# Optimization experiments

Measured on AMD Instinct MI355X. Metric: run time of the kernel, lower is better.

Reference implementation:

```python
import jax, jax.numpy as jnp
import numpy as np

N, P, M, J, H = 32768, 5, 1024, 24, 256
SMPL_THRESH = 0.08


def _rand_transforms(rng, n):
    # random small-angle rotations + small translations -> invertible 4x4 joint transforms
    axis = rng.normal(size=(n, 3))
    axis /= np.linalg.norm(axis, axis=-1, keepdims=True)
    ang = rng.uniform(-0.5, 0.5, size=(n, 1, 1))
    K = np.zeros((n, 3, 3))
    K[:, 0, 1] = -axis[:, 2]; K[:, 0, 2] = axis[:, 1]
    K[:, 1, 0] = axis[:, 2];  K[:, 1, 2] = -axis[:, 0]
    K[:, 2, 0] = -axis[:, 1]; K[:, 2, 1] = axis[:, 0]
    R = np.eye(3)[None] + np.sin(ang) * K + (1.0 - np.cos(ang)) * (K @ K)
    T = np.zeros((n, 4, 4))
    T[:, :3, :3] = R
    T[:, :3, 3] = rng.normal(size=(n, 3)) * 0.1
    T[:, 3, 3] = 1.0
    return T.astype(np.float32)


def setup_inputs() -> dict:
    key = jax.random.key(0)
    ks = jax.random.split(key, 12)
    rng = np.random.default_rng(0)
    pose_pts = jax.random.normal(ks[0], (1, N, 3), jnp.float32) * 0.5
    pose_dirs = jax.random.normal(ks[1], (1, N, 3), jnp.float32)
    pose_dirs = pose_dirs / jnp.linalg.norm(pose_dirs, axis=-1, keepdims=True)
    part_pts = jax.random.normal(ks[2], (P, M, 3), jnp.float32) * 0.5
    part_pbw = jax.nn.softmax(jax.random.normal(ks[3], (P, M, J), jnp.float32), axis=-1)
    A = jnp.asarray(_rand_transforms(rng, J))[None]       # [1,24,4,4]
    big_A = jnp.asarray(_rand_transforms(rng, J))[None]   # [1,24,4,4]
    W1 = jax.random.normal(ks[4], (3, H), jnp.float32) * 0.1
    b1 = jnp.zeros((H,), jnp.float32)
    W2 = jax.random.normal(ks[5], (H, H), jnp.float32) * 0.06
    b2 = jnp.zeros((H,), jnp.float32)
    W3 = jax.random.normal(ks[6], (H, 3), jnp.float32) * 0.06
    b3 = jnp.zeros((3,), jnp.float32)
    lengths2 = jnp.full((P,), M, dtype=jnp.int32)
    return {"pose_pts": pose_pts, "pose_dirs": pose_dirs, "part_pts": part_pts,
            "part_pbw": part_pbw, "A": A, "big_A": big_A,
            "W1": W1, "b1": b1, "W2": W2, "b2": b2, "W3": W3, "b3": b3,
            "lengths2": lengths2}


def _lbs_pipeline(pose_pts, pose_dirs, part_pts, part_pbw, A, big_A,
                  W1, b1, W2, b2, W3, b3, lengths2):
    # ---- KNN (K=1) blend-weight lookup per part (torch.no_grad block) ----
    x = pose_pts[0]                                              # [N,3]
    d2 = (jnp.sum(x * x, -1)[:, None, None]
          - 2.0 * jnp.einsum('nd,pmd->npm', x, part_pts)
          + jnp.sum(part_pts * part_pts, -1)[None])              # [N,P,M]
    valid = jnp.arange(M)[None, :] < lengths2[:, None]           # [P,M]
    d2 = jnp.where(valid[None], jnp.maximum(d2, 0.0), jnp.inf)
    nn = jnp.argmin(d2, axis=-1)                                 # [N,P]
    pnorm = jnp.sqrt(jnp.take_along_axis(d2, nn[..., None], -1)[..., 0])  # [N,P]
    bw = part_pbw[jnp.arange(P)[None, :], nn]                    # [N,P,24]
    bw = jax.lax.stop_gradient(bw)
    pnorm = jax.lax.stop_gradient(pnorm)
    pflag = pnorm < SMPL_THRESH                                  # [N,P]

    # ---- gather-expand: each point assigned to every part ----
    pts_e = jnp.broadcast_to(x[:, None, :], (N, P, 3)).reshape(N * P, 3)
    dirs_e = jnp.broadcast_to(pose_dirs[0][:, None, :], (N, P, 3)).reshape(N * P, 3)
    bw_f = bw.reshape(N * P, J)

    # ---- per-point inverse linear blend skinning ----
    A_bw = jnp.einsum('kj,jxy->kxy', bw_f, A[0])                 # [NP,4,4]
    R_inv = jnp.linalg.inv(A_bw[:, :3, :3])
    tpts = jnp.einsum('kxy,ky->kx', R_inv, pts_e - A_bw[:, :3, 3])
    Ab = jnp.einsum('kj,jxy->kxy', bw_f, big_A[0])               # [NP,4,4]
    Rb = Ab[:, :3, :3]
    init_bigpose = jnp.einsum('kxy,ky->kx', Rb, tpts) + Ab[:, :3, 3]
    tdirs = jnp.einsum('kxy,ky->kx', R_inv, dirs_e)
    tpose_dirs = jnp.einsum('kxy,ky->kx', Rb, tdirs).reshape(1, N, P, 3)

    # ---- tpose deformer (residual MLP, masked by part flag) ----
    h = jax.nn.relu(init_bigpose @ W1 + b1)
    h = jax.nn.relu(h @ W2 + b2)
    resd = 0.05 * jnp.tanh(h @ W3 + b3)
    resd = resd * pflag.reshape(N * P, 1).astype(resd.dtype)
    tpose = (init_bigpose + resd).reshape(1, N, P, 3)
    return (tpose, tpose_dirs, resd.reshape(1, N, P, 3),
            pflag.reshape(1, N, P), init_bigpose[None], pnorm[None])


def reference(pose_pts, pose_dirs, part_pts, part_pbw, A, big_A,
              W1, b1, W2, b2, W3, b3, lengths2):
    return _lbs_pipeline(pose_pts, pose_dirs, part_pts, part_pbw, A, big_A,
                         W1, b1, W2, b2, W3, b3, lengths2)
```

## Files before the change

### kernel.cpp

```cpp
#include <hip/hip_runtime.h>
#include <stdint.h>
#include <math.h>

#define NPTS 32768
#define PP   5
#define MM   1024
#define JJ   24
#define HH   256

#define O0 0
#define O1 491520
#define O2 983040
#define O3 1474560
#define O4 1638400
#define O5 2129920

typedef unsigned short ushort_t;
typedef unsigned int   uint_t;
typedef unsigned long long u64_t;
typedef __attribute__((ext_vector_type(8))) short bf16x8;
typedef __attribute__((ext_vector_type(4))) float f32x4;
typedef __attribute__((ext_vector_type(2))) float f32x2;

__device__ __forceinline__ ushort_t f2bf(float f) {
  union { uint_t i; float f; } v; v.f = f;
  uint_t i = v.i;
  return (ushort_t)((i + 0x7FFFu + ((i >> 16) & 1u)) >> 16);
}
__device__ __forceinline__ uint_t cvt_pk_bf16(float lo, float hi) {
  uint_t r;
  asm("v_cvt_pk_bf16_f32 %0, %1, %2" : "=v"(r) : "v"(lo), "v"(hi));
  return r;
}
__device__ __forceinline__ float tanh_fast(float v) {
  v = fminf(fmaxf(v, -15.f), 15.f);
  float e = __expf(2.f*v);
  return __fdividef(e - 1.f, e + 1.f);
}
__device__ __forceinline__ float dpp_sum16(float x) {
  x += __int_as_float(__builtin_amdgcn_update_dpp(0, __float_as_int(x), 0x108, 0xF, 0xF, true));
  x += __int_as_float(__builtin_amdgcn_update_dpp(0, __float_as_int(x), 0x104, 0xF, 0xF, true));
  x += __int_as_float(__builtin_amdgcn_update_dpp(0, __float_as_int(x), 0x102, 0xF, 0xF, true));
  x += __int_as_float(__builtin_amdgcn_update_dpp(0, __float_as_int(x), 0x101, 0xF, 0xF, true));
  return x;
}

__device__ __forceinline__ void transform_one(
    int n, int p, int nn, float pn, float fl,
    float px, float py, float pz, float dx, float dy, float dz,
    const float* __restrict__ pbw,
    const float4* __restrict__ sA4, const float4* __restrict__ sB4,
    float* __restrict__ out)
{
  const float4* bwr = (const float4*)(pbw + ((size_t)p * MM + nn) * JJ);
  float bw[24];
  #pragma unroll
  for (int q = 0; q < 6; ++q) {
    float4 u = bwr[q];
    bw[q*4+0] = u.x; bw[q*4+1] = u.y; bw[q*4+2] = u.z; bw[q*4+3] = u.w;
  }

  float M1[12], M2[12];
  #pragma unroll
  for (int q = 0; q < 12; ++q) { M1[q] = 0.f; M2[q] = 0.f; }
  #pragma unroll
  for (int j = 0; j < 24; ++j) {
    float w = bw[j];
    float4 a0 = sA4[j*3+0], a1 = sA4[j*3+1], a2 = sA4[j*3+2];
    M1[0]=fmaf(w,a0.x,M1[0]); M1[1]=fmaf(w,a0.y,M1[1]); M1[2]=fmaf(w,a0.z,M1[2]); M1[3]=fmaf(w,a0.w,M1[3]);
    M1[4]=fmaf(w,a1.x,M1[4]); M1[5]=fmaf(w,a1.y,M1[5]); M1[6]=fmaf(w,a1.z,M1[6]); M1[7]=fmaf(w,a1.w,M1[7]);
    M1[8]=fmaf(w,a2.x,M1[8]); M1[9]=fmaf(w,a2.y,M1[9]); M1[10]=fmaf(w,a2.z,M1[10]); M1[11]=fmaf(w,a2.w,M1[11]);
    float4 c0 = sB4[j*3+0], c1 = sB4[j*3+1], c2 = sB4[j*3+2];
    M2[0]=fmaf(w,c0.x,M2[0]); M2[1]=fmaf(w,c0.y,M2[1]); M2[2]=fmaf(w,c0.z,M2[2]); M2[3]=fmaf(w,c0.w,M2[3]);
    M2[4]=fmaf(w,c1.x,M2[4]); M2[5]=fmaf(w,c1.y,M2[5]); M2[6]=fmaf(w,c1.z,M2[6]); M2[7]=fmaf(w,c1.w,M2[7]);
    M2[8]=fmaf(w,c2.x,M2[8]); M2[9]=fmaf(w,c2.y,M2[9]); M2[10]=fmaf(w,c2.z,M2[10]); M2[11]=fmaf(w,c2.w,M2[11]);
  }
  float a=M1[0], b=M1[1], c=M1[2];
  float d=M1[4], e=M1[5], f=M1[6];
  float g=M1[8], h=M1[9], i=M1[10];
  float C00 = e*i - f*h, C01 = c*h - b*i, C02 = b*f - c*e;
  float C10 = f*g - d*i, C11 = a*i - c*g, C12 = c*d - a*f;
  float C20 = d*h - e*g, C21 = b*g - a*h, C22 = a*e - b*d;
  float det = a*C00 + b*C10 + c*C20;
  float rd = 1.0f / det;
  float tx = px - M1[3], ty = py - M1[7], tz = pz - M1[11];
  float t0 = rd * (C00*tx + C01*ty + C02*tz);
  float t1 = rd * (C10*tx + C11*ty + C12*tz);
  float t2 = rd * (C20*tx + C21*ty + C22*tz);
  float i0 = M2[0]*t0 + M2[1]*t1 + M2[2]*t2  + M2[3];
  float i1 = M2[4]*t0 + M2[5]*t1 + M2[6]*t2  + M2[7];
  float i2 = M2[8]*t0 + M2[9]*t1 + M2[10]*t2 + M2[11];
  float d0 = rd * (C00*dx + C01*dy + C02*dz);
  float d1 = rd * (C10*dx + C11*dy + C12*dz);
  float d2 = rd * (C20*dx + C21*dy + C22*dz);
  float e0 = M2[0]*d0 + M2[1]*d1 + M2[2]*d2;
  float e1 = M2[4]*d0 + M2[5]*d1 + M2[6]*d2;
  float e2 = M2[8]*d0 + M2[9]*d1 + M2[10]*d2;

  size_t k = (size_t)n * PP + p;
  out[O1 + k*3+0] = e0; out[O1 + k*3+1] = e1; out[O1 + k*3+2] = e2;
  out[O3 + k] = fl;
  out[O4 + k*3+0] = i0; out[O4 + k*3+1] = i1; out[O4 + k*3+2] = i2;
  out[O5 + k] = pn;
}

__global__ __launch_bounds__(256) void nn_kernel(
    const float* __restrict__ pp0, const float* __restrict__ pp1,
    const float* __restrict__ part_pts, const float* __restrict__ pbw,
    const float* __restrict__ Ag, const float* __restrict__ Bg,
    const int* __restrict__ lengths2,
    const float* __restrict__ W2g, ushort_t* __restrict__ W2bf,
    float* __restrict__ out)
{
  if (blockIdx.x >= 1280) {
    int k = blockIdx.x - 1280;
    int n = threadIdx.x;
    float v = W2g[k*256 + n];
    int kc = k >> 5, quad = (k & 31) >> 3, j = k & 7;
    int tile = n >> 4, lane = quad*16 + (n & 15);
    W2bf[kc*8192 + tile*512 + lane*8 + j] = f2bf(v);
    return;
  }

  __shared__ float4 sXq[256], sYq[256], sZq[256], sWq[256];
  __shared__ float4 sA4[72];
  __shared__ float4 sB4[72];
  int t = threadIdx.x;
  int p  = blockIdx.x >> 8;
  int nb = blockIdx.x & 255;
  int g  = t >> 3;
  int s  = t & 7;
  int n0 = nb*128 + g*4;

  float s0r0 = pp0[0], s0r1 = pp0[1], s0r2 = pp0[2];
  float nrm = s0r0*s0r0 + s0r1*s0r1 + s0r2*s0r2;
  bool c0_is_dirs = fabsf(nrm - 1.0f) < 1e-4f;
  const float* pose_pts  = c0_is_dirs ? pp1 : pp0;
  const float* pose_dirs = c0_is_dirs ? pp0 : pp1;

  {
    #pragma clang fp contract(off)
    float* fX = (float*)sXq; float* fY = (float*)sYq;
    float* fZ = (float*)sZq; float* fW = (float*)sWq;
    for (int i = t; i < MM; i += 256) {
      float x = part_pts[((size_t)p*MM+i)*3+0];
      float y = part_pts[((size_t)p*MM+i)*3+1];
      float z = part_pts[((size_t)p*MM+i)*3+2];
      float yy = ((x*x) + (y*y)) + (z*z);
      fX[i] = x; fY[i] = y; fZ[i] = z; fW[i] = yy;
    }
  }
  for (int i = t; i < 72; i += 256) {
    int l = i*4;
    int j = l / 12, rc = l % 12;
    float4 qa, qb;
    qa.x = Ag[j*16+rc+0]; qa.y = Ag[j*16+rc+1]; qa.z = Ag[j*16+rc+2]; qa.w = Ag[j*16+rc+3];
    qb.x = Bg[j*16+rc+0]; qb.y = Bg[j*16+rc+1]; qb.z = Bg[j*16+rc+2]; qb.w = Bg[j*16+rc+3];
    sA4[i] = qa; sB4[i] = qb;
  }
  int mlen = lengths2[p]; if (mlen > MM) mlen = MM;
  __syncthreads();

  float X[4], Y[4], Z[4];
  f32x2 Xd[4], Yd[4], Zd[4], C2[4];
  {
    #pragma clang fp contract(off)
    const float4* pr = (const float4*)(pose_pts + (size_t)n0*3);
    float4 f0 = pr[0], f1 = pr[1], f2 = pr[2];
    X[0]=f0.x; Y[0]=f0.y; Z[0]=f0.z;
    X[1]=f0.w; Y[1]=f1.x; Z[1]=f1.y;
    X[2]=f1.z; Y[2]=f1.w; Z[2]=f2.x;
    X[3]=f2.y; Y[3]=f2.z; Z[3]=f2.w;
    #pragma unroll
    for (int j = 0; j < 4; ++j) {
      float x2 = ((X[j]*X[j]) + (Y[j]*Y[j])) + (Z[j]*Z[j]);
      Xd[j] = (f32x2){2.0f*X[j], 2.0f*X[j]};
      Yd[j] = (f32x2){2.0f*Y[j], 2.0f*Y[j]};
      Zd[j] = (f32x2){2.0f*Z[j], 2.0f*Z[j]};
      C2[j] = (f32x2){x2, x2};
    }
  }

  float best[4] = {INFINITY, INFINITY, INFINITY, INFINITY};
  int   code[4] = {0, 0, 0, 0};
  {
    #pragma clang fp contract(off)
    int nq = mlen >> 5;
    for (int k = 0; k < nq; ++k) {
      int qi = k*8 + s;
      float4 QX = sXq[qi], QY = sYq[qi], QZ = sZq[qi], QW = sWq[qi];
      f32x2 qx0 = {QX.x, QX.y}, qx1 = {QX.z, QX.w};
      f32x2 qy0 = {QY.x, QY.y}, qy1 = {QY.z, QY.w};
      f32x2 qz0 = {QZ.x, QZ.y}, qz1 = {QZ.z, QZ.w};
      f32x2 qw0 = {QW.x, QW.y}, qw1 = {QW.z, QW.w};
      int cb = k << 2;
      #pragma unroll
      for (int j = 0; j < 4; ++j) {
        f32x2 dt0 = ((Xd[j]*qx0) + (Yd[j]*qy0)) + (Zd[j]*qz0);
        f32x2 tt0 = (C2[j] - dt0) + qw0;
        f32x2 dt1 = ((Xd[j]*qx1) + (Yd[j]*qy1)) + (Zd[j]*qz1);
        f32x2 tt1 = (C2[j] - dt1) + qw1;
        float e0 = fmaxf(tt0.x, 0.f);
        float e1 = fmaxf(tt0.y, 0.f);
        float e2 = fmaxf(tt1.x, 0.f);
        float e3 = fmaxf(tt1.y, 0.f);
        bool l0 = e0 < best[j]; best[j] = fminf(best[j], e0); code[j] = l0 ? cb       : code[j];
        bool l1 = e1 < best[j]; best[j] = fminf(best[j], e1); code[j] = l1 ? (cb | 1) : code[j];
        bool l2 = e2 < best[j]; best[j] = fminf(best[j], e2); code[j] = l2 ? (cb | 2) : code[j];
        bool l3 = e3 < best[j]; best[j] = fminf(best[j], e3); code[j] = l3 ? (cb | 3) : code[j];
      }
    }
    int mb0 = nq << 5;
    if (mb0 < mlen) {
      const float* fX = (const float*)sXq; const float* fY = (const float*)sYq;
      const float* fZ = (const float*)sZq; const float* fW = (const float*)sWq;
      #pragma unroll
      for (int e = 0; e < 4; ++e) {
        int m = mb0 + 4*s + e;
        if (m < mlen) {
          float qx = fX[m], qy = fY[m], qz = fZ[m], qw = fW[m];
          int cc = (nq << 2) | e;
          #pragma unroll
          for (int j = 0; j < 4; ++j) {
            float dt2 = ((Xd[j].x*qx) + (Yd[j].x*qy)) + (Zd[j].x*qz);
            float dd = fmaxf((C2[j].x - dt2) + qw, 0.0f);
            bool lt = dd < best[j];
            best[j] = fminf(best[j], dd);
            code[j] = lt ? cc : code[j];
          }
        }
      }
    }
  }

  u64_t pk[4];
  #pragma unroll
  for (int j = 0; j < 4; ++j) {
    int mj = ((code[j] >> 2) << 5) + 4*s + (code[j] & 3);
    pk[j] = ((u64_t)__float_as_uint(best[j]) << 32) | (uint_t)mj;
    u64_t o;
    o = __shfl_xor(pk[j], 1); if (o < pk[j]) pk[j] = o;
    o = __shfl_xor(pk[j], 2); if (o < pk[j]) pk[j] = o;
    o = __shfl_xor(pk[j], 4); if (o < pk[j]) pk[j] = o;
  }

  if (s < 4) {
    u64_t mypk = (s==0) ? pk[0] : (s==1) ? pk[1] : (s==2) ? pk[2] : pk[3];
    float xa = (s==0) ? X[0] : (s==1) ? X[1] : (s==2) ? X[2] : X[3];
    float ya = (s==0) ? Y[0] : (s==1) ? Y[1] : (s==2) ? Y[2] : Y[3];
    float za = (s==0) ? Z[0] : (s==1) ? Z[1] : (s==2) ? Z[2] : Z[3];
    int n = n0 + s;
    int bm = (int)(mypk & 0xFFFFFFFFull);
    float bd = __uint_as_float((uint_t)(mypk >> 32));
    float pn = sqrtf(bd);
    float fl = ((double)pn < 0.08) ? 1.0f : 0.0f;
    float dxa = pose_dirs[n*3+0], dya = pose_dirs[n*3+1], dza = pose_dirs[n*3+2];
    transform_one(n, p, bm, pn, fl, xa, ya, za, dxa, dya, dza, pbw, sA4, sB4, out);
  }
}

__global__ __launch_bounds__(256) void mlp_kernel(
    const float* __restrict__ W1g, const float* __restrict__ b1g,
    const float* __restrict__ b2g, const float* __restrict__ W3g,
    const float* __restrict__ b3g, const ushort_t* __restrict__ W2bf,
    float* __restrict__ out)
{
  __shared__ ushort_t sH[4*8*512];
  __shared__ float4 w1c[256];
  __shared__ float4 w3b2[256];
  __shared__ float4 sRow[64];
  __shared__ float  pp[64][4][3];

  int t = threadIdx.x;
  int wave = t >> 6, lane = t & 63, quad = lane >> 4, m16 = lane & 15;
  size_t row0 = (size_t)blockIdx.x * 64;

  {
    int c = t;
    w1c[c]  = make_float4(W1g[c], W1g[256+c], W1g[512+c], b1g[c]);
    w3b2[c] = make_float4(W3g[c*3+0], W3g[c*3+1], W3g[c*3+2], b2g[c]);
    if (t < 64) {
      size_t r = row0 + t;
      sRow[t] = make_float4(out[O4 + r*3+0], out[O4 + r*3+1], out[O4 + r*3+2], 0.f);
    }
  }
  __syncthreads();

  {
    int q8 = t & 31, rg = t >> 5;
    int kcw = q8 >> 2, qd = q8 & 3;
    int c0 = kcw*32 + qd*8;
    float4 wv[8];
    #pragma unroll
    for (int j = 0; j < 8; ++j) wv[j] = w1c[c0 + j];
    #pragma unroll
    for (int rr = 0; rr < 8; ++rr) {
      int r = rg*8 + rr;
      float4 xyz = sRow[r];
      uint_t u0, u1, u2, u3;
      {
        float4 wA = wv[0], wB = wv[1];
        float hA = fmaxf(fmaf(xyz.z, wA.z, fmaf(xyz.y, wA.y, fmaf(xyz.x, wA.x, wA.w))), 0.f);
        float hB = fmaxf(fmaf(xyz.z, wB.z, fmaf(xyz.y, wB.y, fmaf(xyz.x, wB.x, wB.w))), 0.f);
        u0 = cvt_pk_bf16(hA, hB);
      }
      {
        float4 wA = wv[2], wB = wv[3];
        float hA = fmaxf(fmaf(xyz.z, wA.z, fmaf(xyz.y, wA.y, fmaf(xyz.x, wA.x, wA.w))), 0.f);
        float hB = fmaxf(fmaf(xyz.z, wB.z, fmaf(xyz.y, wB.y, fmaf(xyz.x, wB.x, wB.w))), 0.f);
        u1 = cvt_pk_bf16(hA, hB);
      }
      {
        float4 wA = wv[4], wB = wv[5];
        float hA = fmaxf(fmaf(xyz.z, wA.z, fmaf(xyz.y, wA.y, fmaf(xyz.x, wA.x, wA.w))), 0.f);
        float hB = fmaxf(fmaf(xyz.z, wB.z, fmaf(xyz.y, wB.y, fmaf(xyz.x, wB.x, wB.w))), 0.f);
        u2 = cvt_pk_bf16(hA, hB);
      }
      {
        float4 wA = wv[6], wB = wv[7];
        float hA = fmaxf(fmaf(xyz.z, wA.z, fmaf(xyz.y, wA.y, fmaf(xyz.x, wA.x, wA.w))), 0.f);
        float hB = fmaxf(fmaf(xyz.z, wB.z, fmaf(xyz.y, wB.y, fmaf(xyz.x, wB.x, wB.w))), 0.f);
        u3 = cvt_pk_bf16(hA, hB);
      }
      int mt = r >> 4, l = qd*16 + (r & 15);
      *(uint4*)(&sH[((mt*8 + kcw)*64 + l)*8]) = make_uint4(u0, u1, u2, u3);
    }
  }
  __syncthreads();

  const ushort_t* Wlane = W2bf + (size_t)wave*2048 + lane*8;
  bf16x8 Bcur[4], Bnxt[4];
  #pragma unroll
  for (int q = 0; q < 4; ++q) Bcur[q] = *(const bf16x8*)(Wlane + q*512);

  f32x4 acc[16];
  #pragma unroll
  for (int i = 0; i < 16; ++i) acc[i] = (f32x4){0.f,0.f,0.f,0.f};

  #pragma unroll 1
  for (int kc = 0; kc < 8; ++kc) {
    bf16x8 Af[4];
    #pragma unroll
    for (int mt = 0; mt < 4; ++mt)
      Af[mt] = *(const bf16x8*)(&sH[((mt*8 + kc)*64 + lane)*8]);
    if (kc < 7) {
      #pragma unroll
      for (int q = 0; q < 4; ++q)
        Bnxt[q] = *(const bf16x8*)(Wlane + (kc+1)*8192 + q*512);
    }
    #pragma unroll
    for (int mt = 0; mt < 4; ++mt)
      #pragma unroll
      for (int q = 0; q < 4; ++q)
        acc[mt*4+q] = __builtin_amdgcn_mfma_f32_16x16x32_bf16(Af[mt], Bcur[q], acc[mt*4+q], 0, 0, 0);
    if (kc < 7) {
      #pragma unroll
      for (int q = 0; q < 4; ++q) Bcur[q] = Bnxt[q];
    }
  }

  float4 cvq[4];
  #pragma unroll
  for (int q = 0; q < 4; ++q) cvq[q] = w3b2[(wave*4+q)*16 + m16];

  #pragma unroll
  for (int mt = 0; mt < 4; ++mt) {
    #pragma unroll
    for (int reg = 0; reg < 4; ++reg) {
      float p0 = 0.f, p1 = 0.f, p2 = 0.f;
      #pragma unroll
      for (int q = 0; q < 4; ++q) {
        float h2 = fmaxf(acc[mt*4+q][reg] + cvq[q].w, 0.f);
        p0 = fmaf(h2, cvq[q].x, p0);
        p1 = fmaf(h2, cvq[q].y, p1);
        p2 = fmaf(h2, cvq[q].z, p2);
      }
      p0 = dpp_sum16(p0);
      p1 = dpp_sum16(p1);
      p2 = dpp_sum16(p2);
      if (m16 == 0) {
        int lr = mt*16 + quad*4 + reg;
        pp[lr][wave][0] = p0;
        pp[lr][wave][1] = p1;
        pp[lr][wave][2] = p2;
      }
    }
  }
  __syncthreads();

  {
    int lr = t >> 2, c = t & 3;
    if (c < 3) {
      float v = ((pp[lr][0][c] + pp[lr][1][c]) + pp[lr][2][c]) + pp[lr][3][c];
      size_t r = row0 + lr;
      float fl = out[O3 + r];
      float iv = out[O4 + r*3 + c];
      float rr = 0.05f * tanh_fast(v + b3g[c]) * fl;
      out[O0 + r*3 + c] = iv + rr;
      out[O2 + r*3 + c] = rr;
    }
  }
}

extern "C" void kernel_launch(void* const* d_in, const int* in_sizes, int n_in,
                              void* d_out, int out_size, void* d_ws, size_t ws_size,
                              hipStream_t stream) {
  (void)out_size; (void)ws_size;
  const int want[13] = {98304, 98304, 15360, 122880, 384, 384, 768, 256, 65536, 256, 768, 3, 5};
  int idx[13];
  bool used[64] = {false};
  for (int L = 0; L < 13; ++L) {
    idx[L] = -1;
    for (int s = 0; s < n_in && s < 64; ++s) {
      if (!used[s] && in_sizes[s] == want[L]) { idx[L] = s; used[s] = true; break; }
    }
    if (idx[L] < 0) idx[L] = L;
  }
  const float* pp0       = (const float*)d_in[idx[0]];
  const float* pp1       = (const float*)d_in[idx[1]];
  const float* part_pts  = (const float*)d_in[idx[2]];
  const float* part_pbw  = (const float*)d_in[idx[3]];
  const float* A         = (const float*)d_in[idx[4]];
  const float* bigA      = (const float*)d_in[idx[5]];
  const float* W1        = (const float*)d_in[idx[6]];
  const float* b1        = (const float*)d_in[idx[7]];
  const float* W2        = (const float*)d_in[idx[8]];
  const float* b2        = (const float*)d_in[idx[9]];
  const float* W3        = (const float*)d_in[idx[10]];
  const float* b3        = (const float*)d_in[idx[11]];
  const int*   lengths2  = (const int*)d_in[idx[12]];
  float* out = (float*)d_out;
  ushort_t* W2bf = (ushort_t*)d_ws;

  nn_kernel<<<1536, 256, 0, stream>>>(pp0, pp1, part_pts, part_pbw,
                                      A, bigA, lengths2, W2, W2bf, out);
  mlp_kernel<<<2560, 256, 0, stream>>>(W1, b1, b2, W3, b3, W2bf, out);
}
```

Before: 168.9 us.

## Fuse NN/LBS kernel with residual MLP, keep transformed points in LDS

Merges the KNN/skinning kernel and the MLP kernel into one kernel per 128-point tile. The transformed bigpose points and flags are kept in shared memory and fed straight into two 64-row MLP chunks, so they are no longer re-read from global memory and one kernel boundary goes away. It also splits the W2 bf16 conversion into a separate small launch, unions the shared-memory buffers of the two phases, and XOR-swizzles the sH layout to reduce LDS bank conflicts. The cost is that MLP work now runs serially inside the larger block, which may lower occupancy and overlap.

```diff
diff --git a/kernel.cpp b/kernel.cpp
--- a/kernel.cpp
+++ b/kernel.cpp
@@ -45,12 +45,23 @@
   return x;
 }
 
+__global__ __launch_bounds__(256) void prep_w2(const float* __restrict__ W2g,
+                                               ushort_t* __restrict__ W2bf)
+{
+  int k = blockIdx.x;
+  int n = threadIdx.x;
+  float v = W2g[k*256 + n];
+  int kc = k >> 5, quad = (k & 31) >> 3, j = k & 7;
+  int tile = n >> 4, lane = quad*16 + (n & 15);
+  W2bf[kc*8192 + tile*512 + lane*8 + j] = f2bf(v);
+}
+
 __device__ __forceinline__ void transform_one(
     int n, int p, int nn, float pn, float fl,
     float px, float py, float pz, float dx, float dy, float dz,
     const float* __restrict__ pbw,
     const float4* __restrict__ sA4, const float4* __restrict__ sB4,
-    float* __restrict__ out)
+    float* __restrict__ out, float4* __restrict__ sib)
 {
   const float4* bwr = (const float4*)(pbw + ((size_t)p * MM + nn) * JJ);
   float bw[24];
@@ -102,29 +113,35 @@
   out[O3 + k] = fl;
   out[O4 + k*3+0] = i0; out[O4 + k*3+1] = i1; out[O4 + k*3+2] = i2;
   out[O5 + k] = pn;
-}
-
-__global__ __launch_bounds__(256) void nn_kernel(
+  *sib = make_float4(i0, i1, i2, fl);
+}
+
+struct P1 {
+  float4 sXq[256], sYq[256], sZq[256], sWq[256];
+  float4 sA4[72], sB4[72];
+};
+struct P2 {
+  ushort_t sH[4*8*512];
+  float4 w1c[256];
+  float4 w3b2[256];
+  float  prt[64][4][3];
+};
+
+__global__ __launch_bounds__(256) void fused_kernel(
     const float* __restrict__ pp0, const float* __restrict__ pp1,
     const float* __restrict__ part_pts, const float* __restrict__ pbw,
     const float* __restrict__ Ag, const float* __restrict__ Bg,
     const int* __restrict__ lengths2,
-    const float* __restrict__ W2g, ushort_t* __restrict__ W2bf,
+    const float* __restrict__ W1g, const float* __restrict__ b1g,
+    const float* __restrict__ b2g, const float* __restrict__ W3g,
+    const float* __restrict__ b3g, const ushort_t* __restrict__ W2bf,
     float* __restrict__ out)
 {
-  if (blockIdx.x >= 1280) {
-    int k = blockIdx.x - 1280;
-    int n = threadIdx.x;
-    float v = W2g[k*256 + n];
-    int kc = k >> 5, quad = (k & 31) >> 3, j = k & 7;
-    int tile = n >> 4, lane = quad*16 + (n & 15);
-    W2bf[kc*8192 + tile*512 + lane*8 + j] = f2bf(v);
-    return;
-  }
-
-  __shared__ float4 sXq[256], sYq[256], sZq[256], sWq[256];
-  __shared__ float4 sA4[72];
-  __shared__ float4 sB4[72];
+  __shared__ __align__(16) char smem_raw[sizeof(P2)];
+  __shared__ float4 sIB[128];
+  P1& p1 = *reinterpret_cast<P1*>(smem_raw);
+  P2& p2 = *reinterpret_cast<P2*>(smem_raw);
+
   int t = threadIdx.x;
   int p  = blockIdx.x >> 8;
   int nb = blockIdx.x & 255;
@@ -140,8 +157,8 @@
 
   {
     #pragma clang fp contract(off)
-    float* fX = (float*)sXq; float* fY = (float*)sYq;
-    float* fZ = (float*)sZq; float* fW = (float*)sWq;
+    float* fX = (float*)p1.sXq; float* fY = (float*)p1.sYq;
+    float* fZ = (float*)p1.sZq; float* fW = (float*)p1.sWq;
     for (int i = t; i < MM; i += 256) {
       float x = part_pts[((size_t)p*MM+i)*3+0];
       float y = part_pts[((size_t)p*MM+i)*3+1];
@@ -156,7 +173,7 @@
     float4 qa, qb;
     qa.x = Ag[j*16+rc+0]; qa.y = Ag[j*16+rc+1]; qa.z = Ag[j*16+rc+2]; qa.w = Ag[j*16+rc+3];
     qb.x = Bg[j*16+rc+0]; qb.y = Bg[j*16+rc+1]; qb.z = Bg[j*16+rc+2]; qb.w = Bg[j*16+rc+3];
-    sA4[i] = qa; sB4[i] = qb;
+    p1.sA4[i] = qa; p1.sB4[i] = qb;
   }
   int mlen = lengths2[p]; if (mlen > MM) mlen = MM;
   __syncthreads();
@@ -188,7 +205,7 @@
     int nq = mlen >> 5;
     for (int k = 0; k < nq; ++k) {
       int qi = k*8 + s;
-      float4 QX = sXq[qi], QY = sYq[qi], QZ = sZq[qi], QW = sWq[qi];
+      float4 QX = p1.sXq[qi], QY = p1.sYq[qi], QZ = p1.sZq[qi], QW = p1.sWq[qi];
       f32x2 qx0 = {QX.x, QX.y}, qx1 = {QX.z, QX.w};
       f32x2 qy0 = {QY.x, QY.y}, qy1 = {QY.z, QY.w};
       f32x2 qz0 = {QZ.x, QZ.y}, qz1 = {QZ.z, QZ.w};
@@ -212,8 +229,8 @@
     }
     int mb0 = nq << 5;
     if (mb0 < mlen) {
-      const float* fX = (const float*)sXq; const float* fY = (const float*)sYq;
-      const float* fZ = (const float*)sZq; const float* fW = (const float*)sWq;
+      const float* fX = (const float*)p1.sXq; const float* fY = (const float*)p1.sYq;
+      const float* fZ = (const float*)p1.sZq; const float* fW = (const float*)p1.sWq;
       #pragma unroll
       for (int e = 0; e < 4; ++e) {
         int m = mb0 + 4*s + e;
@@ -255,150 +272,139 @@
     float pn = sqrtf(bd);
     float fl = ((double)pn < 0.08) ? 1.0f : 0.0f;
     float dxa = pose_dirs[n*3+0], dya = pose_dirs[n*3+1], dza = pose_dirs[n*3+2];
-    transform_one(n, p, bm, pn, fl, xa, ya, za, dxa, dya, dza, pbw, sA4, sB4, out);
-  }
-}
-
-__global__ __launch_bounds__(256) void mlp_kernel(
-    const float* __restrict__ W1g, const float* __restrict__ b1g,
-    const float* __restrict__ b2g, const float* __restrict__ W3g,
-    const float* __restrict__ b3g, const ushort_t* __restrict__ W2bf,
-    float* __restrict__ out)
-{
-  __shared__ ushort_t sH[4*8*512];
-  __shared__ float4 w1c[256];
-  __shared__ float4 w3b2[256];
-  __shared__ float4 sRow[64];
-  __shared__ float  pp[64][4][3];
-
-  int t = threadIdx.x;
+    transform_one(n, p, bm, pn, fl, xa, ya, za, dxa, dya, dza, pbw,
+                  p1.sA4, p1.sB4, out, &sIB[g*4 + s]);
+  }
+  __syncthreads();
+
   int wave = t >> 6, lane = t & 63, quad = lane >> 4, m16 = lane & 15;
-  size_t row0 = (size_t)blockIdx.x * 64;
-
   {
     int c = t;
-    w1c[c]  = make_float4(W1g[c], W1g[256+c], W1g[512+c], b1g[c]);
-    w3b2[c] = make_float4(W3g[c*3+0], W3g[c*3+1], W3g[c*3+2], b2g[c]);
-    if (t < 64) {
-      size_t r = row0 + t;
-      sRow[t] = make_float4(out[O4 + r*3+0], out[O4 + r*3+1], out[O4 + r*3+2], 0.f);
-    }
+    p2.w1c[c]  = make_float4(W1g[c], W1g[256+c], W1g[512+c], b1g[c]);
+    p2.w3b2[c] = make_float4(W3g[c*3+0], W3g[c*3+1], W3g[c*3+2], b2g[c]);
   }
   __syncthreads();
 
-  {
-    int q8 = t & 31, rg = t >> 5;
-    int kcw = q8 >> 2, qd = q8 & 3;
-    int c0 = kcw*32 + qd*8;
-    float4 wv[8];
+  #pragma unroll 1
+  for (int ch = 0; ch < 2; ++ch) {
+    {
+      int q8 = t & 31, rg = t >> 5;
+      int kcw = q8 >> 2, qd = q8 & 3;
+      int c0 = kcw*32 + qd*8;
+      float4 wv[8];
+      #pragma unroll
+      for (int j = 0; j < 8; ++j) wv[j] = p2.w1c[c0 + j];
+      #pragma unroll
+      for (int rr = 0; rr < 8; ++rr) {
+        int r = rg*8 + rr;
+        float4 xyz = sIB[ch*64 + r];
+        uint_t u0, u1, u2, u3;
+        {
+          float4 wA = wv[0], wB = wv[1];
+          float hA = fmaxf(fmaf(xyz.z, wA.z, fmaf(xyz.y, wA.y, fmaf(xyz.x, wA.x, wA.w))), 0.f);
+          float hB = fmaxf(fmaf(xyz.z, wB.z, fmaf(xyz.y, wB.y, fmaf(xyz.x, wB.x, wB.w))), 0.f);
+          u0 = cvt_pk_bf16(hA, hB);
+        }
+        {
+          float4 wA = wv[2], wB = wv[3];
+          float hA = fmaxf(fmaf(xyz.z, wA.z, fmaf(xyz.y, wA.y, fmaf(xyz.x, wA.x, wA.w))), 0.f);
+          float hB = fmaxf(fmaf(xyz.z, wB.z, fmaf(xyz.y, wB.y, fmaf(xyz.x, wB.x, wB.w))), 0.f);
+          u1 = cvt_pk_bf16(hA, hB);
+        }
+        {
+          float4 wA = wv[4], wB = wv[5];
+          float hA = fmaxf(fmaf(xyz.z, wA.z, fmaf(xyz.y, wA.y, fmaf(xyz.x, wA.x, wA.w))), 0.f);
+          float hB = fmaxf(fmaf(xyz.z, wB.z, fmaf(xyz.y, wB.y, fmaf(xyz.x, wB.x, wB.w))), 0.f);
+          u2 = cvt_pk_bf16(hA, hB);
+        }
+        {
+          float4 wA = wv[6], wB = wv[7];
+          float hA = fmaxf(fmaf(xyz.z, wA.z, fmaf(xyz.y, wA.y, fmaf(xyz.x, wA.x, wA.w))), 0.f);
+          float hB = fmaxf(fmaf(xyz.z, wB.z, fmaf(xyz.y, wB.y, fmaf(xyz.x, wB.x, wB.w))), 0.f);
+          u3 = cvt_pk_bf16(hA, hB);
+        }
+        int mt = r >> 4, r15 = r & 15;
+        int l = qd*16 + (r15 ^ kcw);
+        *(uint4*)(&p2.sH[((mt*8 + kcw)*64 + l)*8]) = make_uint4(u0, u1, u2, u3);
+      }
+    }
+    __syncthreads();
+
+    const ushort_t* Wlane = W2bf + (size_t)wave*2048 + lane*8;
+    bf16x8 Bcur[4], Bnxt[4];
     #pragma unroll
-    for (int j = 0; j < 8; ++j) wv[j] = w1c[c0 + j];
+    for (int q = 0; q < 4; ++q) Bcur[q] = *(const bf16x8*)(Wlane + q*512);
+
+    f32x4 acc[16];
     #pragma unroll
-    for (int rr = 0; rr < 8; ++rr) {
-      int r = rg*8 + rr;
-      float4 xyz = sRow[r];
-      uint_t u0, u1, u2, u3;
-      {
-        float4 wA = wv[0], wB = wv[1];
-        float hA = fmaxf(fmaf(xyz.z, wA.z, fmaf(xyz.y, wA.y, fmaf(xyz.x, wA.x, wA.w))), 0.f);
-        float hB = fmaxf(fmaf(xyz.z, wB.z, fmaf(xyz.y, wB.y, fmaf(xyz.x, wB.x, wB.w))), 0.f);
-        u0 = cvt_pk_bf16(hA, hB);
-      }
-      {
-        float4 wA = wv[2], wB = wv[3];
-        float hA = fmaxf(fmaf(xyz.z, wA.z, fmaf(xyz.y, wA.y, fmaf(xyz.x, wA.x, wA.w))), 0.f);
-        float hB = fmaxf(fmaf(xyz.z, wB.z, fmaf(xyz.y, wB.y, fmaf(xyz.x, wB.x, wB.w))), 0.f);
-        u1 = cvt_pk_bf16(hA, hB);
-      }
-      {
-        float4 wA = wv[4], wB = wv[5];
-        float hA = fmaxf(fmaf(xyz.z, wA.z, fmaf(xyz.y, wA.y, fmaf(xyz.x, wA.x, wA.w))), 0.f);
-        float hB = fmaxf(fmaf(xyz.z, wB.z, fmaf(xyz.y, wB.y, fmaf(xyz.x, wB.x, wB.w))), 0.f);
-        u2 = cvt_pk_bf16(hA, hB);
-      }
-      {
-        float4 wA = wv[6], wB = wv[7];
-        float hA = fmaxf(fmaf(xyz.z, wA.z, fmaf(xyz.y, wA.y, fmaf(xyz.x, wA.x, wA.w))), 0.f);
-        float hB = fmaxf(fmaf(xyz.z, wB.z, fmaf(xyz.y, wB.y, fmaf(xyz.x, wB.x, wB.w))), 0.f);
-        u3 = cvt_pk_bf16(hA, hB);
-      }
-      int mt = r >> 4, l = qd*16 + (r & 15);
-      *(uint4*)(&sH[((mt*8 + kcw)*64 + l)*8]) = make_uint4(u0, u1, u2, u3);
-    }
-  }
-  __syncthreads();
-
-  const ushort_t* Wlane = W2bf + (size_t)wave*2048 + lane*8;
-  bf16x8 Bcur[4], Bnxt[4];
-  #pragma unroll
-  for (int q = 0; q < 4; ++q) Bcur[q] = *(const bf16x8*)(Wlane + q*512);
-
-  f32x4 acc[16];
-  #pragma unroll
-  for (int i = 0; i < 16; ++i) acc[i] = (f32x4){0.f,0.f,0.f,0.f};
-
-  #pragma unroll 1
-  for (int kc = 0; kc < 8; ++kc) {
-    bf16x8 Af[4];
+    for (int i = 0; i < 16; ++i) acc[i] = (f32x4){0.f,0.f,0.f,0.f};
+
+    #pragma unroll 1
+    for (int kc = 0; kc < 8; ++kc) {
+      bf16x8 Af[4];
+      int lslot = quad*16 + (m16 ^ kc);
+      #pragma unroll
+      for (int mt = 0; mt < 4; ++mt)
+        Af[mt] = *(const bf16x8*)(&p2.sH[((mt*8 + kc)*64 + lslot)*8]);
+      if (kc < 7) {
+        #pragma unroll
+        for (int q = 0; q < 4; ++q)
+          Bnxt[q] = *(const bf16x8*)(Wlane + (kc+1)*8192 + q*512);
+      }
+      #pragma unroll
+      for (int mt = 0; mt < 4; ++mt)
+        #pragma unroll
+        for (int q = 0; q < 4; ++q)
+          acc[mt*4+q] = __builtin_amdgcn_mfma_f32_16x16x32_bf16(Af[mt], Bcur[q], acc[mt*4+q], 0, 0, 0);
+      if (kc < 7) {
+        #pragma unroll
+        for (int q = 0; q < 4; ++q) Bcur[q] = Bnxt[q];
+      }
+    }
+
+    float4 cvq[4];
     #pragma unroll
-    for (int mt = 0; mt < 4; ++mt)
-      Af[mt] = *(const bf16x8*)(&sH[((mt*8 + kc)*64 + lane)*8]);
-    if (kc < 7) {
-      #pragma unroll
-      for (int q = 0; q < 4; ++q)
-        Bnxt[q] = *(const bf16x8*)(Wlane + (kc+1)*8192 + q*512);
-    }
+    for (int q = 0; q < 4; ++q) cvq[q] = p2.w3b2[(wave*4+q)*16 + m16];
+
     #pragma unroll
-    for (int mt = 0; mt < 4; ++mt)
-      #pragma unroll
-      for (int q = 0; q < 4; ++q)
-        acc[mt*4+q] = __builtin_amdgcn_mfma_f32_16x16x32_bf16(Af[mt], Bcur[q], acc[mt*4+q], 0, 0, 0);
-    if (kc < 7) {
-      #pragma unroll
-      for (int q = 0; q < 4; ++q) Bcur[q] = Bnxt[q];
-    }
-  }
-
-  float4 cvq[4];
-  #pragma unroll
-  for (int q = 0; q < 4; ++q) cvq[q] = w3b2[(wave*4+q)*16 + m16];
-
-  #pragma unroll
-  for (int mt = 0; mt < 4; ++mt) {
-    #pragma unroll
-    for (int reg = 0; reg < 4; ++reg) {
-      float p0 = 0.f, p1 = 0.f, p2 = 0.f;
-      #pragma unroll
-      for (int q = 0; q < 4; ++q) {
-        float h2 = fmaxf(acc[mt*4+q][reg] + cvq[q].w, 0.f);
-        p0 = fmaf(h2, cvq[q].x, p0);
-        p1 = fmaf(h2, cvq[q].y, p1);
-        p2 = fmaf(h2, cvq[q].z, p2);
-      }
-      p0 = dpp_sum16(p0);
-      p1 = dpp_sum16(p1);
-      p2 = dpp_sum16(p2);
-      if (m16 == 0) {
-        int lr = mt*16 + quad*4 + reg;
-        pp[lr][wave][0] = p0;
-        pp[lr][wave][1] = p1;
-        pp[lr][wave][2] = p2;
-      }
-    }
-  }
-  __syncthreads();
-
-  {
-    int lr = t >> 2, c = t & 3;
-    if (c < 3) {
-      float v = ((pp[lr][0][c] + pp[lr][1][c]) + pp[lr][2][c]) + pp[lr][3][c];
-      size_t r = row0 + lr;
-      float fl = out[O3 + r];
-      float iv = out[O4 + r*3 + c];
-      float rr = 0.05f * tanh_fast(v + b3g[c]) * fl;
-      out[O0 + r*3 + c] = iv + rr;
-      out[O2 + r*3 + c] = rr;
-    }
+    for (int mt = 0; mt < 4; ++mt) {
+      #pragma unroll
+      for (int reg = 0; reg < 4; ++reg) {
+        float q0 = 0.f, q1 = 0.f, q2 = 0.f;
+        #pragma unroll
+        for (int q = 0; q < 4; ++q) {
+          float h2 = fmaxf(acc[mt*4+q][reg] + cvq[q].w, 0.f);
+          q0 = fmaf(h2, cvq[q].x, q0);
+          q1 = fmaf(h2, cvq[q].y, q1);
+          q2 = fmaf(h2, cvq[q].z, q2);
+        }
+        q0 = dpp_sum16(q0);
+        q1 = dpp_sum16(q1);
+        q2 = dpp_sum16(q2);
+        if (m16 == 0) {
+          int lr = mt*16 + quad*4 + reg;
+          p2.prt[lr][wave][0] = q0;
+          p2.prt[lr][wave][1] = q1;
+          p2.prt[lr][wave][2] = q2;
+        }
+      }
+    }
+    __syncthreads();
+
+    {
+      int lr = t >> 2, c = t & 3;
+      if (c < 3) {
+        float v = ((p2.prt[lr][0][c] + p2.prt[lr][1][c]) + p2.prt[lr][2][c]) + p2.prt[lr][3][c];
+        int n = nb*128 + ch*64 + lr;
+        size_t k = (size_t)n * PP + p;
+        float4 ib = sIB[ch*64 + lr];
+        float iv = (c == 0) ? ib.x : (c == 1) ? ib.y : ib.z;
+        float rr = 0.05f * tanh_fast(v + b3g[c]) * ib.w;
+        out[O0 + k*3 + c] = iv + rr;
+        out[O2 + k*3 + c] = rr;
+      }
+    }
+    __syncthreads();
   }
 }
 
@@ -432,7 +438,8 @@
   float* out = (float*)d_out;
   ushort_t* W2bf = (ushort_t*)d_ws;
 
-  nn_kernel<<<1536, 256, 0, stream>>>(pp0, pp1, part_pts, part_pbw,
-                                      A, bigA, lengths2, W2, W2bf, out);
-  mlp_kernel<<<2560, 256, 0, stream>>>(W1, b1, b2, W3, b3, W2bf, out);
-}
+  prep_w2<<<256, 256, 0, stream>>>(W2, W2bf);
+  fused_kernel<<<1280, 256, 0, stream>>>(pp0, pp1, part_pts, part_pbw,
+                                         A, bigA, lengths2,
+                                         W1, b1, b2, W3, b3, W2bf, out);
+}
```

Result: no change. 171.1 us (+1.3%).

## Split MLP block into two 32-row passes and prefetch KNN query tiles

Applied to the files above, without the earlier changes.

The MLP kernel now handles its 64 rows in two passes of 32 rows. This halves the accumulator registers and shrinks shared memory by aliasing the partial-sum buffer onto the hidden-activation buffer, with the aim of raising occupancy. The flag and intermediate point are cached in shared memory, so they are no longer re-read from global memory in the epilogue. Separately, the KNN loop software-prefetches the next query float4s from LDS to hide latency. The cost is more barriers per block, and each W2 fragment is now loaded twice from global or L2.

```diff
diff --git a/kernel.cpp b/kernel.cpp
--- a/kernel.cpp
+++ b/kernel.cpp
@@ -186,28 +186,34 @@
   {
     #pragma clang fp contract(off)
     int nq = mlen >> 5;
-    for (int k = 0; k < nq; ++k) {
-      int qi = k*8 + s;
-      float4 QX = sXq[qi], QY = sYq[qi], QZ = sZq[qi], QW = sWq[qi];
-      f32x2 qx0 = {QX.x, QX.y}, qx1 = {QX.z, QX.w};
-      f32x2 qy0 = {QY.x, QY.y}, qy1 = {QY.z, QY.w};
-      f32x2 qz0 = {QZ.x, QZ.y}, qz1 = {QZ.z, QZ.w};
-      f32x2 qw0 = {QW.x, QW.y}, qw1 = {QW.z, QW.w};
-      int cb = k << 2;
-      #pragma unroll
-      for (int j = 0; j < 4; ++j) {
-        f32x2 dt0 = ((Xd[j]*qx0) + (Yd[j]*qy0)) + (Zd[j]*qz0);
-        f32x2 tt0 = (C2[j] - dt0) + qw0;
-        f32x2 dt1 = ((Xd[j]*qx1) + (Yd[j]*qy1)) + (Zd[j]*qz1);
-        f32x2 tt1 = (C2[j] - dt1) + qw1;
-        float e0 = fmaxf(tt0.x, 0.f);
-        float e1 = fmaxf(tt0.y, 0.f);
-        float e2 = fmaxf(tt1.x, 0.f);
-        float e3 = fmaxf(tt1.y, 0.f);
-        bool l0 = e0 < best[j]; best[j] = fminf(best[j], e0); code[j] = l0 ? cb       : code[j];
-        bool l1 = e1 < best[j]; best[j] = fminf(best[j], e1); code[j] = l1 ? (cb | 1) : code[j];
-        bool l2 = e2 < best[j]; best[j] = fminf(best[j], e2); code[j] = l2 ? (cb | 2) : code[j];
-        bool l3 = e3 < best[j]; best[j] = fminf(best[j], e3); code[j] = l3 ? (cb | 3) : code[j];
+    if (nq > 0) {
+      float4 QX = sXq[s], QY = sYq[s], QZ = sZq[s], QW = sWq[s];
+      for (int k = 0; k < nq; ++k) {
+        int kn = (k + 1 < nq) ? (k + 1) : 0;
+        int qn = kn*8 + s;
+        float4 NX = sXq[qn], NY = sYq[qn], NZ = sZq[qn], NW = sWq[qn];
+
+        f32x2 qx0 = {QX.x, QX.y}, qx1 = {QX.z, QX.w};
+        f32x2 qy0 = {QY.x, QY.y}, qy1 = {QY.z, QY.w};
+        f32x2 qz0 = {QZ.x, QZ.y}, qz1 = {QZ.z, QZ.w};
+        f32x2 qw0 = {QW.x, QW.y}, qw1 = {QW.z, QW.w};
+        int cb = k << 2;
+        #pragma unroll
+        for (int j = 0; j < 4; ++j) {
+          f32x2 dt0 = ((Xd[j]*qx0) + (Yd[j]*qy0)) + (Zd[j]*qz0);
+          f32x2 tt0 = (C2[j] - dt0) + qw0;
+          f32x2 dt1 = ((Xd[j]*qx1) + (Yd[j]*qy1)) + (Zd[j]*qz1);
+          f32x2 tt1 = (C2[j] - dt1) + qw1;
+          float e0 = fmaxf(tt0.x, 0.f);
+          float e1 = fmaxf(tt0.y, 0.f);
+          float e2 = fmaxf(tt1.x, 0.f);
+          float e3 = fmaxf(tt1.y, 0.f);
+          bool l0 = e0 < best[j]; best[j] = fminf(best[j], e0); code[j] = l0 ? cb       : code[j];
+          bool l1 = e1 < best[j]; best[j] = fminf(best[j], e1); code[j] = l1 ? (cb | 1) : code[j];
+          bool l2 = e2 < best[j]; best[j] = fminf(best[j], e2); code[j] = l2 ? (cb | 2) : code[j];
+          bool l3 = e3 < best[j]; best[j] = fminf(best[j], e3); code[j] = l3 ? (cb | 3) : code[j];
+        }
+        QX = NX; QY = NY; QZ = NZ; QW = NW;
       }
     }
     int mb0 = nq << 5;
@@ -265,11 +271,12 @@
     const float* __restrict__ b3g, const ushort_t* __restrict__ W2bf,
     float* __restrict__ out)
 {
-  __shared__ ushort_t sH[4*8*512];
-  __shared__ float4 w1c[256];
-  __shared__ float4 w3b2[256];
-  __shared__ float4 sRow[64];
-  __shared__ float  pp[64][4][3];
+  __shared__ __align__(16) char smem[25088];
+  ushort_t* sH   = (ushort_t*)smem;
+  float4*   w1c  = (float4*)(smem + 16384);
+  float4*   w3b2 = (float4*)(smem + 20480);
+  float4*   sRow = (float4*)(smem + 24576);
+  float*    prt  = (float*)smem;
 
   int t = threadIdx.x;
   int wave = t >> 6, lane = t & 63, quad = lane >> 4, m16 = lane & 15;
@@ -279,126 +286,135 @@
     int c = t;
     w1c[c]  = make_float4(W1g[c], W1g[256+c], W1g[512+c], b1g[c]);
     w3b2[c] = make_float4(W3g[c*3+0], W3g[c*3+1], W3g[c*3+2], b2g[c]);
-    if (t < 64) {
-      size_t r = row0 + t;
-      sRow[t] = make_float4(out[O4 + r*3+0], out[O4 + r*3+1], out[O4 + r*3+2], 0.f);
-    }
-  }
-  __syncthreads();
-
-  {
-    int q8 = t & 31, rg = t >> 5;
-    int kcw = q8 >> 2, qd = q8 & 3;
-    int c0 = kcw*32 + qd*8;
-    float4 wv[8];
+  }
+
+  #pragma unroll 1
+  for (int pass = 0; pass < 2; ++pass) {
+    size_t rbase = row0 + pass*32;
+    if (t < 32) {
+      size_t r = rbase + t;
+      sRow[t] = make_float4(out[O4 + r*3+0], out[O4 + r*3+1], out[O4 + r*3+2],
+                            out[O3 + r]);
+    }
+    __syncthreads();
+
+    {
+      int q8 = t & 31, rg = t >> 5;
+      int kcw = q8 >> 2, qd = q8 & 3;
+      int c0 = kcw*32 + qd*8;
+      float4 wv[8];
+      #pragma unroll
+      for (int j = 0; j < 8; ++j) wv[j] = w1c[c0 + j];
+      #pragma unroll
+      for (int rr = 0; rr < 4; ++rr) {
+        int r = rg*4 + rr;
+        float4 xyz = sRow[r];
+        uint_t u0, u1, u2, u3;
+        {
+          float4 wA = wv[0], wB = wv[1];
+          float hA = fmaxf(fmaf(xyz.z, wA.z, fmaf(xyz.y, wA.y, fmaf(xyz.x, wA.x, wA.w))), 0.f);
+          float hB = fmaxf(fmaf(xyz.z, wB.z, fmaf(xyz.y, wB.y, fmaf(xyz.x, wB.x, wB.w))), 0.f);
+          u0 = cvt_pk_bf16(hA, hB);
+        }
+        {
+          float4 wA = wv[2], wB = wv[3];
+          float hA = fmaxf(fmaf(xyz.z, wA.z, fmaf(xyz.y, wA.y, fmaf(xyz.x, wA.x, wA.w))), 0.f);
+          float hB = fmaxf(fmaf(xyz.z, wB.z, fmaf(xyz.y, wB.y, fmaf(xyz.x, wB.x, wB.w))), 0.f);
+          u1 = cvt_pk_bf16(hA, hB);
+        }
+        {
+          float4 wA = wv[4], wB = wv[5];
+          float hA = fmaxf(fmaf(xyz.z, wA.z, fmaf(xyz.y, wA.y, fmaf(xyz.x, wA.x, wA.w))), 0.f);
+          float hB = fmaxf(fmaf(xyz.z, wB.z, fmaf(xyz.y, wB.y, fmaf(xyz.x, wB.x, wB.w))), 0.f);
+          u2 = cvt_pk_bf16(hA, hB);
+        }
+        {
+          float4 wA = wv[6], wB = wv[7];
+          float hA = fmaxf(fmaf(xyz.z, wA.z, fmaf(xyz.y, wA.y, fmaf(xyz.x, wA.x, wA.w))), 0.f);
+          float hB = fmaxf(fmaf(xyz.z, wB.z, fmaf(xyz.y, wB.y, fmaf(xyz.x, wB.x, wB.w))), 0.f);
+          u3 = cvt_pk_bf16(hA, hB);
+        }
+        int mt = r >> 4, r15 = r & 15;
+        int l = qd*16 + r15;
+        *(uint4*)(&sH[((mt*8 + kcw)*64 + l)*8]) = make_uint4(u0, u1, u2, u3);
+      }
+    }
+    __syncthreads();
+
+    const ushort_t* Wlane = W2bf + (size_t)wave*2048 + lane*8;
+    bf16x8 Bcur[4], Bnxt[4];
     #pragma unroll
-    for (int j = 0; j < 8; ++j) wv[j] = w1c[c0 + j];
+    for (int q = 0; q < 4; ++q) Bcur[q] = *(const bf16x8*)(Wlane + q*512);
+
+    f32x4 acc[8];
     #pragma unroll
-    for (int rr = 0; rr < 8; ++rr) {
-      int r = rg*8 + rr;
-      float4 xyz = sRow[r];
-      uint_t u0, u1, u2, u3;
-      {
-        float4 wA = wv[0], wB = wv[1];
-        float hA = fmaxf(fmaf(xyz.z, wA.z, fmaf(xyz.y, wA.y, fmaf(xyz.x, wA.x, wA.w))), 0.f);
-        float hB = fmaxf(fmaf(xyz.z, wB.z, fmaf(xyz.y, wB.y, fmaf(xyz.x, wB.x, wB.w))), 0.f);
-        u0 = cvt_pk_bf16(hA, hB);
-      }
-      {
-        float4 wA = wv[2], wB = wv[3];
-        float hA = fmaxf(fmaf(xyz.z, wA.z, fmaf(xyz.y, wA.y, fmaf(xyz.x, wA.x, wA.w))), 0.f);
-        float hB = fmaxf(fmaf(xyz.z, wB.z, fmaf(xyz.y, wB.y, fmaf(xyz.x, wB.x, wB.w))), 0.f);
-        u1 = cvt_pk_bf16(hA, hB);
-      }
-      {
-        float4 wA = wv[4], wB = wv[5];
-        float hA = fmaxf(fmaf(xyz.z, wA.z, fmaf(xyz.y, wA.y, fmaf(xyz.x, wA.x, wA.w))), 0.f);
-        float hB = fmaxf(fmaf(xyz.z, wB.z, fmaf(xyz.y, wB.y, fmaf(xyz.x, wB.x, wB.w))), 0.f);
-        u2 = cvt_pk_bf16(hA, hB);
-      }
-      {
-        float4 wA = wv[6], wB = wv[7];
-        float hA = fmaxf(fmaf(xyz.z, wA.z, fmaf(xyz.y, wA.y, fmaf(xyz.x, wA.x, wA.w))), 0.f);
-        float hB = fmaxf(fmaf(xyz.z, wB.z, fmaf(xyz.y, wB.y, fmaf(xyz.x, wB.x, wB.w))), 0.f);
-        u3 = cvt_pk_bf16(hA, hB);
-      }
-      int mt = r >> 4, l = qd*16 + (r & 15);
-      *(uint4*)(&sH[((mt*8 + kcw)*64 + l)*8]) = make_uint4(u0, u1, u2, u3);
-    }
-  }
-  __syncthreads();
-
-  const ushort_t* Wlane = W2bf + (size_t)wave*2048 + lane*8;
-  bf16x8 Bcur[4], Bnxt[4];
-  #pragma unroll
-  for (int q = 0; q < 4; ++q) Bcur[q] = *(const bf16x8*)(Wlane + q*512);
-
-  f32x4 acc[16];
-  #pragma unroll
-  for (int i = 0; i < 16; ++i) acc[i] = (f32x4){0.f,0.f,0.f,0.f};
-
-  #pragma unroll 1
-  for (int kc = 0; kc < 8; ++kc) {
-    bf16x8 Af[4];
+    for (int i = 0; i < 8; ++i) acc[i] = (f32x4){0.f,0.f,0.f,0.f};
+
+    #pragma unroll 1
+    for (int kc = 0; kc < 8; ++kc) {
+      bf16x8 Af[2];
+      #pragma unroll
+      for (int mt = 0; mt < 2; ++mt)
+        Af[mt] = *(const bf16x8*)(&sH[((mt*8 + kc)*64 + lane)*8]);
+      if (kc < 7) {
+        #pragma unroll
+        for (int q = 0; q < 4; ++q)
+          Bnxt[q] = *(const bf16x8*)(Wlane + (kc+1)*8192 + q*512);
+      }
+      #pragma unroll
+      for (int mt = 0; mt < 2; ++mt)
+        #pragma unroll
+        for (int q = 0; q < 4; ++q)
+          acc[mt*4+q] = __builtin_amdgcn_mfma_f32_16x16x32_bf16(Af[mt], Bcur[q], acc[mt*4+q], 0, 0, 0);
+      if (kc < 7) {
+        #pragma unroll
+        for (int q = 0; q < 4; ++q) Bcur[q] = Bnxt[q];
+      }
+    }
+    __syncthreads();
+
+    float4 cvq[4];
     #pragma unroll
-    for (int mt = 0; mt < 4; ++mt)
-      Af[mt] = *(const bf16x8*)(&sH[((mt*8 + kc)*64 + lane)*8]);
-    if (kc < 7) {
-      #pragma unroll
-      for (int q = 0; q < 4; ++q)
-        Bnxt[q] = *(const bf16x8*)(Wlane + (kc+1)*8192 + q*512);
-    }
+    for (int q = 0; q < 4; ++q) cvq[q] = w3b2[(wave*4+q)*16 + m16];
+
     #pragma unroll
-    for (int mt = 0; mt < 4; ++mt)
-      #pragma unroll
-      for (int q = 0; q < 4; ++q)
-        acc[mt*4+q] = __builtin_amdgcn_mfma_f32_16x16x32_bf16(Af[mt], Bcur[q], acc[mt*4+q], 0, 0, 0);
-    if (kc < 7) {
-      #pragma unroll
-      for (int q = 0; q < 4; ++q) Bcur[q] = Bnxt[q];
-    }
-  }
-
-  float4 cvq[4];
-  #pragma unroll
-  for (int q = 0; q < 4; ++q) cvq[q] = w3b2[(wave*4+q)*16 + m16];
-
-  #pragma unroll
-  for (int mt = 0; mt < 4; ++mt) {
-    #pragma unroll
-    for (int reg = 0; reg < 4; ++reg) {
-      float p0 = 0.f, p1 = 0.f, p2 = 0.f;
-      #pragma unroll
-      for (int q = 0; q < 4; ++q) {
-        float h2 = fmaxf(acc[mt*4+q][reg] + cvq[q].w, 0.f);
-        p0 = fmaf(h2, cvq[q].x, p0);
-        p1 = fmaf(h2, cvq[q].y, p1);
-        p2 = fmaf(h2, cvq[q].z, p2);
-      }
-      p0 = dpp_sum16(p0);
-      p1 = dpp_sum16(p1);
-      p2 = dpp_sum16(p2);
-      if (m16 == 0) {
-        int lr = mt*16 + quad*4 + reg;
-        pp[lr][wave][0] = p0;
-        pp[lr][wave][1] = p1;
-        pp[lr][wave][2] = p2;
-      }
-    }
-  }
-  __syncthreads();
-
-  {
-    int lr = t >> 2, c = t & 3;
-    if (c < 3) {
-      float v = ((pp[lr][0][c] + pp[lr][1][c]) + pp[lr][2][c]) + pp[lr][3][c];
-      size_t r = row0 + lr;
-      float fl = out[O3 + r];
-      float iv = out[O4 + r*3 + c];
-      float rr = 0.05f * tanh_fast(v + b3g[c]) * fl;
-      out[O0 + r*3 + c] = iv + rr;
-      out[O2 + r*3 + c] = rr;
-    }
+    for (int mt = 0; mt < 2; ++mt) {
+      #pragma unroll
+      for (int reg = 0; reg < 4; ++reg) {
+        float q0 = 0.f, q1 = 0.f, q2 = 0.f;
+        #pragma unroll
+        for (int q = 0; q < 4; ++q) {
+          float h2 = fmaxf(acc[mt*4+q][reg] + cvq[q].w, 0.f);
+          q0 = fmaf(h2, cvq[q].x, q0);
+          q1 = fmaf(h2, cvq[q].y, q1);
+          q2 = fmaf(h2, cvq[q].z, q2);
+        }
+        q0 = dpp_sum16(q0);
+        q1 = dpp_sum16(q1);
+        q2 = dpp_sum16(q2);
+        if (m16 == 0) {
+          int lr = mt*16 + quad*4 + reg;
+          prt[(lr*4 + wave)*3 + 0] = q0;
+          prt[(lr*4 + wave)*3 + 1] = q1;
+          prt[(lr*4 + wave)*3 + 2] = q2;
+        }
+      }
+    }
+    __syncthreads();
+
+    if (t < 128) {
+      int lr = t >> 2, c = t & 3;
+      if (c < 3) {
+        float v = ((prt[(lr*4+0)*3+c] + prt[(lr*4+1)*3+c]) + prt[(lr*4+2)*3+c]) + prt[(lr*4+3)*3+c];
+        size_t r = rbase + lr;
+        float4 ib = sRow[lr];
+        float iv = (c == 0) ? ib.x : (c == 1) ? ib.y : ib.z;
+        float rr = 0.05f * tanh_fast(v + b3g[c]) * ib.w;
+        out[O0 + r*3 + c] = iv + rr;
+        out[O2 + r*3 + c] = rr;
+      }
+    }
+    __syncthreads();
   }
 }
 
```

New measurement: 171.1 us. No clear change (+1.2%).
